# Performance work log

Measured on AMD Instinct MI355X. Metric: run time of the kernel, lower is better.

## Reference

```python
import jax, jax.numpy as jnp
from jax import lax
import numpy as np

B, T, A = 128, 2048, 3
H = 100  # LSTM units
F = 64   # conv filters


def setup_inputs() -> dict:
    key = jax.random.key(0)
    ks = jax.random.split(key, 8)
    s = lambda k, shape, scale: (jax.random.normal(k, shape, dtype=jnp.float32) * scale)
    return {
        "state_input": s(ks[0], (B, T, 1), 1.0),
        "conv_w": s(ks[1], (2, 1, F), 0.5),
        "conv_b": jnp.zeros((F,), jnp.float32),
        "lstm1_w": s(ks[2], (F, 4 * H), 0.08),
        "lstm1_u": s(ks[3], (H, 4 * H), 0.08),
        "lstm1_b": jnp.zeros((4 * H,), jnp.float32),
        "lstm2_w": s(ks[4], (H, 4 * H), 0.08),
        "lstm2_u": s(ks[5], (H, 4 * H), 0.08),
        "lstm2_b": jnp.zeros((4 * H,), jnp.float32),
        "dense_w": s(ks[6], (H, A), 0.1),
        "dense_b": jnp.zeros((A,), jnp.float32),
    }


def _lstm_relu(x, W, U, b, return_sequences):
    # Keras LSTM with activation='relu', recurrent_activation='sigmoid'.
    # Gate order: i, f, g(candidate), o. h = o * relu(c).
    Bz = x.shape[0]
    xz = jnp.einsum("btf,fg->btg", x, W) + b  # precompute input projections [B,T,4H]
    h0 = jnp.zeros((Bz, U.shape[0]), x.dtype)
    c0 = jnp.zeros_like(h0)

    def step(carry, xz_t):
        h, c = carry
        z = xz_t + h @ U
        i, f, g, o = jnp.split(z, 4, axis=-1)
        i = jax.nn.sigmoid(i)
        f = jax.nn.sigmoid(f)
        g = jax.nn.relu(g)
        o = jax.nn.sigmoid(o)
        c = f * c + i * g
        h = o * jax.nn.relu(c)
        return (h, c), (h if return_sequences else 0.0)

    (h_last, _), hs = lax.scan(step, (h0, c0), jnp.swapaxes(xz, 0, 1))
    if return_sequences:
        return jnp.swapaxes(hs, 0, 1)  # [B,T,H]
    return h_last


def reference(state_input, conv_w, conv_b, lstm1_w, lstm1_u, lstm1_b,
              lstm2_w, lstm2_u, lstm2_b, dense_w, dense_b):
    # Conv1D(filters=64, kernel_size=2, padding='valid', relu): [B,T,1]->[B,T-1,64]
    x = lax.conv_general_dilated(
        state_input, conv_w, window_strides=(1,), padding="VALID",
        dimension_numbers=("NWC", "WIO", "NWC"))
    x = jax.nn.relu(x + conv_b)
    # MaxPool1D(pool_size=1) is the identity.
    x = _lstm_relu(x, lstm1_w, lstm1_u, lstm1_b, return_sequences=True)
    # Dropout at inference is identity.
    x = _lstm_relu(x, lstm2_w, lstm2_u, lstm2_b, return_sequences=False)  # [B,H]
    logits = x @ dense_w + dense_b
    return jax.nn.softmax(logits, axis=-1)
```

## Files before the change

### kernel.cpp

```cpp
#include <hip/hip_runtime.h>
#include <math.h>


typedef _Float16 h2 __attribute__((ext_vector_type(2)));

#define TT 2048
#define TP 2047
#define HH 100
#define G4 400
#define FF 64
#define NB 128

#define K1 192
#define QC 112
#define NPH2 (400 * 96)
#define NCH2 (400 * 112)
#define CHK 64
#define NCHUNK 32
#define RINGC 4
#define CHUNK_DW (CHK * 50)

#define WS_FLAGS (NPH2 + NCH2)
#define WS_RING  (WS_FLAGS + 256)

#define L24(X) X(0) X(1) X(2) X(3) X(4) X(5) X(6) X(7) X(8) X(9) \
 X(10) X(11) X(12) X(13) X(14) X(15) X(16) X(17) X(18) X(19) \
 X(20) X(21) X(22) X(23)
#define L28(X) L24(X) X(24) X(25) X(26) X(27)

#define FD(w, x, acc) acc = __builtin_amdgcn_fdot2(w, x, acc, false)
#define B2(f) __builtin_bit_cast(h2, f)

#define DW4(i) h2 wa##i, wb##i, wc##i, wd##i;
#define LPK(i) { const float4 v = gptr[i]; \
  wa##i = B2(v.x); wb##i = B2(v.y); wc##i = B2(v.z); wd##i = B2(v.w); }

#define DOTP(r, i0, i1, i2, i3) { const float4 v = vb[r]; \
  const h2 x0 = B2(v.x), x1 = B2(v.y), x2 = B2(v.z), x3 = B2(v.w); \
  FD(wa##i0, x0, zA0); FD(wb##i0, x0, zB0); FD(wc##i0, x0, zC0); FD(wd##i0, x0, zD0); \
  FD(wa##i1, x1, zA1); FD(wb##i1, x1, zB1); FD(wc##i1, x1, zC1); FD(wd##i1, x1, zD1); \
  FD(wa##i2, x2, zA0); FD(wb##i2, x2, zB0); FD(wc##i2, x2, zC0); FD(wd##i2, x2, zD0); \
  FD(wa##i3, x3, zA1); FD(wb##i3, x3, zB1); FD(wc##i3, x3, zC1); FD(wd##i3, x3, zD1); }

static __device__ __forceinline__ float qsum4(float z) {
    int p1 = __builtin_amdgcn_update_dpp(0, __builtin_bit_cast(int, z),
                                         0xB1, 0xF, 0xF, true);
    float s1 = z + __builtin_bit_cast(float, p1);
    int p2 = __builtin_amdgcn_update_dpp(0, __builtin_bit_cast(int, s1),
                                         0x4E, 0xF, 0xF, true);
    return s1 + __builtin_bit_cast(float, p2);
}
static __device__ __forceinline__ float sig(float z) {
    return 1.0f / (1.0f + __expf(-z));
}

static __device__ __forceinline__ _Float16 pwv(const float* __restrict__ W,
                                               const float* __restrict__ U,
                                               int c, int k) {
    float v = (k < FF) ? W[k * G4 + c] : (k < FF + HH ? U[(k - FF) * G4 + c] : 0.0f);
    return (_Float16)v;
}
static __device__ __forceinline__ _Float16 cwv2(const float* __restrict__ W,
                                                const float* __restrict__ U,
                                                int c, int k) {
    if (k < 112) return (k < HH) ? (_Float16)W[k * G4 + c] : (_Float16)0.0f;
    const int kk = k - 112;
    return (kk < HH) ? (_Float16)U[kk * G4 + c] : (_Float16)0.0f;
}

__global__ void prep_weights(const float* __restrict__ w1, const float* __restrict__ u1,
                             const float* __restrict__ w2, const float* __restrict__ u2,
                             h2* __restrict__ ws)
{
    const int idx = blockIdx.x * 256 + threadIdx.x;
    if (idx >= NPH2 + NCH2) return;
    _Float16 lo, hi;
    if (idx < NPH2) {
        const int rt = idx / 96, r = idx % 96;
        const int q = r >> 2, g = r & 3;
        const int p = rt >> 2, sq = rt & 3;
        const int c = g * HH + p;
        const int k = sq * 48 + 2 * q;
        lo = pwv(w1, u1, c, k); hi = pwv(w1, u1, c, k + 1);
    } else {
        const int j = idx - NPH2;
        const int rt = j / 112, r = j % 112;
        const int i = r >> 2, g = r & 3;
        const int p = rt >> 2, sq = rt & 3;
        const int c = g * HH + p;
        const int k = 56 * sq + 2 * i;
        lo = cwv2(w2, u2, c, k); hi = cwv2(w2, u2, c, k + 1);
    }
    ws[idx] = h2{lo, hi};
}

__global__ __launch_bounds__(512, 2)
void fused_lstm_kernel(const float* __restrict__ s,
                       const float* __restrict__ conv_w,
                       const float* __restrict__ conv_b,
                       const float* __restrict__ b1,
                       const float* __restrict__ b2,
                       const float* __restrict__ dw, const float* __restrict__ db,
                       h2* __restrict__ wpk,
                       float* __restrict__ out)
{
    const int tid  = threadIdx.x;
    const int bb   = blockIdx.x;
    const int b    = bb & (NB - 1);
    const bool prod = bb < NB;

    int* pflag = (int*)(wpk + WS_FLAGS) + b;
    int* aflag = (int*)(wpk + WS_FLAGS) + 128 + b;
    unsigned* ring = (unsigned*)(wpk + WS_RING) + (size_t)b * (RINGC * CHUNK_DW);

    __shared__ float s_buf[TT];
    __shared__ __align__(16) _Float16 X1[2 * K1];
    __shared__ __align__(16) _Float16 CB[CHK * QC];
    __shared__ __align__(16) _Float16 HR[2 * QC];

    if (prod) {
        for (int i = tid; i < TT; i += 512) s_buf[i] = s[(size_t)b * TT + i];
        if (tid < 2 * K1) X1[tid] = (_Float16)0.0f;
    } else {
        if (tid < CHK * 6) {
            const int row = tid / 6, ii = 50 + tid % 6;
            ((unsigned*)CB)[row * 56 + ii] = 0u;
        }
        if (tid < QC) ((unsigned*)HR)[tid] = 0u;
    }
    __syncthreads();

    if (prod) {
        if (tid < 448) {
            const int rt = tid;
            const int active = rt < 400;
            const int lrt = active ? rt : 0;
            const int p = lrt >> 2, sq = lrt & 3;
            const int cA = p, cBi = HH + p, cC = 2 * HH + p, cD = 3 * HH + p;
            const int kb = sq * 48;

            const float4* gptr = (const float4*)(wpk + (size_t)lrt * 96);
            L24(DW4)
            L24(LPK)
            const float bA = b1[cA], bB = b1[cBi], bC = b1[cC], bD = b1[cD];
            __syncthreads();

            float c = 0.0f;
            for (int t = 0; t < TP; ++t) {
                if ((t & 63) == 0) {
                    const int k = t >> 6;
                    if (tid == 0 && k >= RINGC) {
                        int g = 0;
                        while (__hip_atomic_load(aflag, __ATOMIC_ACQUIRE,
                                                 __HIP_MEMORY_SCOPE_AGENT) < k - (RINGC - 1)
                               && g < 50000000) { ++g; __builtin_amdgcn_s_sleep(8); }
                    }
                    __syncthreads();
                }
                if (active) {
                    _Float16* cur = X1 + (t & 1) * K1;
                    _Float16* nx1 = X1 + ((t & 1) ^ 1) * K1;
                    float zA0 = 0.f, zA1 = 0.f, zB0 = 0.f, zB1 = 0.f;
                    float zC0 = 0.f, zC1 = 0.f, zD0 = 0.f, zD1 = 0.f;
                    const float4* vb = (const float4*)(cur + kb);
                    DOTP(0, 0, 1, 2, 3)     DOTP(1, 4, 5, 6, 7)
                    DOTP(2, 8, 9, 10, 11)   DOTP(3, 12, 13, 14, 15)
                    DOTP(4, 16, 17, 18, 19) DOTP(5, 20, 21, 22, 23)
                    const float zi = qsum4(zA0 + zA1) + bA;
                    const float zf = qsum4(zB0 + zB1) + bB;
                    const float zg = qsum4(zC0 + zC1) + bC;
                    const float zo = qsum4(zD0 + zD1) + bD;
                    c = fmaf(sig(zf), c, sig(zi) * fmaxf(zg, 0.f));
                    const float h = sig(zo) * fmaxf(c, 0.f);
                    if (sq == 0) {
                        const _Float16 hq = (_Float16)h;
                        nx1[FF + p] = hq;
                        const unsigned hb = (unsigned)__builtin_bit_cast(unsigned short, hq);
                        const unsigned prt =
                            (unsigned)__builtin_amdgcn_ds_swizzle((int)hb, 0x101F) & 0xFFFFu;
                        if (!(p & 1)) {
                            const unsigned dwv = hb | (prt << 16);
                            __hip_atomic_store(ring + ((t >> 6) & 3) * CHUNK_DW
                                                    + (t & 63) * 50 + (p >> 1),
                                               dwv, __ATOMIC_RELAXED,
                                               __HIP_MEMORY_SCOPE_AGENT);
                        }
                    }
                    if (((t & 63) == 63) || (t == TP - 1))
                        asm volatile("s_waitcnt vmcnt(0)" ::: "memory");
                }
                __syncthreads();
                if (tid == 0 && (((t & 63) == 63) || (t == TP - 1)))
                    __hip_atomic_fetch_add(pflag, 1, __ATOMIC_RELEASE,
                                           __HIP_MEMORY_SCOPE_AGENT);
            }
        } else {
            const int f = tid - 448;
            const float cv0 = conv_w[f], cv1 = conv_w[FF + f], cb0 = conv_b[f];
            X1[f] = (_Float16)fmaxf(fmaf(s_buf[0], cv0, fmaf(s_buf[1], cv1, cb0)), 0.f);
            __syncthreads();
            for (int t = 0; t < TP; ++t) {
                if ((t & 63) == 0) __syncthreads();
                if (t + 1 < TP) {
                    _Float16* nx1 = X1 + ((t & 1) ^ 1) * K1;
                    nx1[f] = (_Float16)fmaxf(
                        fmaf(s_buf[t + 1], cv0, fmaf(s_buf[t + 2], cv1, cb0)), 0.f);
                }
                __syncthreads();
            }
        }
    } else {
        if (tid < 448) {
            const int rt = tid;
            const int active = rt < 400;
            const int lrt = active ? rt : 0;
            const int p = lrt >> 2, sq = lrt & 3;
            const int cA = p, cBi = HH + p, cC = 2 * HH + p, cD = 3 * HH + p;

            const float4* gptr = (const float4*)(wpk + NPH2 + (size_t)lrt * 112);
            L28(DW4)
            L28(LPK)
            const float bA = b2[cA], bB = b2[cBi], bC = b2[cC], bD = b2[cD];
            __syncthreads();

            float c = 0.0f;
            for (int k = 0; k < NCHUNK; ++k) {
                if (tid == 0) {
                    int g = 0;
                    while (__hip_atomic_load(pflag, __ATOMIC_ACQUIRE,
                                             __HIP_MEMORY_SCOPE_AGENT) < k + 1
                           && g < 50000000) { ++g; __builtin_amdgcn_s_sleep(8); }
                }
                __syncthreads();
                const int csz = (TP - (k << 6) < CHK) ? (TP - (k << 6)) : CHK;
                unsigned* gsrc = ring + (k & 3) * CHUNK_DW;
                for (int d = tid; d < csz * 50; d += 448)
                    ((unsigned*)CB)[(d / 50) * 56 + (d % 50)] =
                        __hip_atomic_load(gsrc + d, __ATOMIC_RELAXED,
                                          __HIP_MEMORY_SCOPE_AGENT);
                __syncthreads();
                if (tid == 0)
                    __hip_atomic_fetch_add(aflag, 1, __ATOMIC_RELAXED,
                                           __HIP_MEMORY_SCOPE_AGENT);
                for (int lt = 0; lt < csz; ++lt) {
                    const int t = (k << 6) + lt;
                    if (active) {
                        const _Float16* ob = (sq < 2)
                            ? (CB + lt * QC + sq * 56)
                            : (HR + (t & 1) * QC + (sq - 2) * 56);
                        float zA0 = 0.f, zA1 = 0.f, zB0 = 0.f, zB1 = 0.f;
                        float zC0 = 0.f, zC1 = 0.f, zD0 = 0.f, zD1 = 0.f;
                        const float4* vb = (const float4*)ob;
                        DOTP(0, 0, 1, 2, 3)     DOTP(1, 4, 5, 6, 7)
                        DOTP(2, 8, 9, 10, 11)   DOTP(3, 12, 13, 14, 15)
                        DOTP(4, 16, 17, 18, 19) DOTP(5, 20, 21, 22, 23)
                        DOTP(6, 24, 25, 26, 27)
                        const float zi = qsum4(zA0 + zA1) + bA;
                        const float zf = qsum4(zB0 + zB1) + bB;
                        const float zg = qsum4(zC0 + zC1) + bC;
                        const float zo = qsum4(zD0 + zD1) + bD;
                        c = fmaf(sig(zf), c, sig(zi) * fmaxf(zg, 0.f));
                        const float h = sig(zo) * fmaxf(c, 0.f);
                        if (sq == 0)
                            HR[((t & 1) ^ 1) * QC + p] = (_Float16)h;
                    }
                    __syncthreads();
                }
            }

            if (rt == 0) {
                float l[3];
#pragma unroll
                for (int a = 0; a < 3; ++a) {
                    float acc = db[a];
                    for (int j = 0; j < HH; ++j)
                        acc = fmaf((float)HR[QC + j], dw[j * 3 + a], acc);
                    l[a] = acc;
                }
                const float m = fmaxf(l[0], fmaxf(l[1], l[2]));
                const float e0 = __expf(l[0] - m), e1 = __expf(l[1] - m), e2 = __expf(l[2] - m);
                const float inv = 1.0f / (e0 + e1 + e2);
                out[b * 3 + 0] = e0 * inv;
                out[b * 3 + 1] = e1 * inv;
                out[b * 3 + 2] = e2 * inv;
            }
        } else {
            __syncthreads();
            for (int k = 0; k < NCHUNK; ++k) {
                __syncthreads();
                const int csz = (TP - (k << 6) < CHK) ? (TP - (k << 6)) : CHK;
                __syncthreads();
                for (int lt = 0; lt < csz; ++lt)
                    __syncthreads();
            }
        }
    }
}

extern "C" void kernel_launch(void* const* d_in, const int* in_sizes, int n_in,
                              void* d_out, int out_size, void* d_ws, size_t ws_size,
                              hipStream_t stream) {
    const float* s      = (const float*)d_in[0];
    const float* conv_w = (const float*)d_in[1];
    const float* conv_b = (const float*)d_in[2];
    const float* w1     = (const float*)d_in[3];
    const float* u1     = (const float*)d_in[4];
    const float* b1     = (const float*)d_in[5];
    const float* w2     = (const float*)d_in[6];
    const float* u2     = (const float*)d_in[7];
    const float* b2     = (const float*)d_in[8];
    const float* dw     = (const float*)d_in[9];
    const float* db     = (const float*)d_in[10];

    h2* ws = (h2*)d_ws;
    hipMemsetAsync((void*)((int*)(ws + WS_FLAGS)), 0, 256 * sizeof(int), stream);
    const int nh2 = NPH2 + NCH2;
    prep_weights<<<(nh2 + 255) / 256, 256, 0, stream>>>(w1, u1, w2, u2, ws);
    fused_lstm_kernel<<<256, 512, 0, stream>>>(
        s, conv_w, conv_b, b1, b2, dw, db, ws, (float*)d_out);
}
```

Baseline: 1.879 ms.

## Precompute per-chunk input projections and give each thread one full gate row

Both LSTM layers now compute the input projection for a whole 32-step chunk in parallel into shared memory, leaving only the recurrent h@U dot in the serial loop. Each thread now owns one full gate column instead of a quarter of the K range for four gates, and DPP lane swaps gather the four gate values instead of reducing partial sums. The conv is computed per chunk rather than streamed by a dedicated warp group. In exchange, each thread holds 104 packed weight registers, shared memory grows to about 57 KB, and the chunk size halves, doubling producer/consumer flag handshakes.

Result: slower. 2.371 ms (+26.2%).

```diff
diff --git a/kernel.cpp b/kernel.cpp
--- a/kernel.cpp
+++ b/kernel.cpp
@@ -11,61 +11,31 @@
 #define FF 64
 #define NB 128
 
-#define K1 192
-#define QC 112
-#define NPH2 (400 * 96)
-#define NCH2 (400 * 112)
-#define CHK 64
-#define NCHUNK 32
+#define CHK 32
+#define NCHUNK 64
 #define RINGC 4
 #define CHUNK_DW (CHK * 50)
 
-#define WS_FLAGS (NPH2 + NCH2)
+#define NPW (400 * 84)
+#define NCW (400 * 104)
+#define WS_FLAGS (NPW + NCW)
 #define WS_RING  (WS_FLAGS + 256)
 
-#define L24(X) X(0) X(1) X(2) X(3) X(4) X(5) X(6) X(7) X(8) X(9) \
- X(10) X(11) X(12) X(13) X(14) X(15) X(16) X(17) X(18) X(19) \
- X(20) X(21) X(22) X(23)
-#define L28(X) L24(X) X(24) X(25) X(26) X(27)
-
-#define FD(w, x, acc) acc = __builtin_amdgcn_fdot2(w, x, acc, false)
+#define FD2(w, xs, acc) acc = __builtin_amdgcn_fdot2(w, xs, acc, false)
 #define B2(f) __builtin_bit_cast(h2, f)
 
-#define DW4(i) h2 wa##i, wb##i, wc##i, wd##i;
-#define LPK(i) { const float4 v = gptr[i]; \
-  wa##i = B2(v.x); wb##i = B2(v.y); wc##i = B2(v.z); wd##i = B2(v.w); }
-
-#define DOTP(r, i0, i1, i2, i3) { const float4 v = vb[r]; \
-  const h2 x0 = B2(v.x), x1 = B2(v.y), x2 = B2(v.z), x3 = B2(v.w); \
-  FD(wa##i0, x0, zA0); FD(wb##i0, x0, zB0); FD(wc##i0, x0, zC0); FD(wd##i0, x0, zD0); \
-  FD(wa##i1, x1, zA1); FD(wb##i1, x1, zB1); FD(wc##i1, x1, zC1); FD(wd##i1, x1, zD1); \
-  FD(wa##i2, x2, zA0); FD(wb##i2, x2, zB0); FD(wc##i2, x2, zC0); FD(wd##i2, x2, zD0); \
-  FD(wa##i3, x3, zA1); FD(wb##i3, x3, zB1); FD(wc##i3, x3, zC1); FD(wd##i3, x3, zD1); }
-
-static __device__ __forceinline__ float qsum4(float z) {
-    int p1 = __builtin_amdgcn_update_dpp(0, __builtin_bit_cast(int, z),
-                                         0xB1, 0xF, 0xF, true);
-    float s1 = z + __builtin_bit_cast(float, p1);
-    int p2 = __builtin_amdgcn_update_dpp(0, __builtin_bit_cast(int, s1),
-                                         0x4E, 0xF, 0xF, true);
-    return s1 + __builtin_bit_cast(float, p2);
+static __device__ __forceinline__ float xswap1(float z) {
+    int p = __builtin_amdgcn_update_dpp(0, __builtin_bit_cast(int, z),
+                                        0xB1, 0xF, 0xF, true);
+    return __builtin_bit_cast(float, p);
+}
+static __device__ __forceinline__ float xswap2(float z) {
+    int p = __builtin_amdgcn_update_dpp(0, __builtin_bit_cast(int, z),
+                                        0x4E, 0xF, 0xF, true);
+    return __builtin_bit_cast(float, p);
 }
 static __device__ __forceinline__ float sig(float z) {
     return 1.0f / (1.0f + __expf(-z));
-}
-
-static __device__ __forceinline__ _Float16 pwv(const float* __restrict__ W,
-                                               const float* __restrict__ U,
-                                               int c, int k) {
-    float v = (k < FF) ? W[k * G4 + c] : (k < FF + HH ? U[(k - FF) * G4 + c] : 0.0f);
-    return (_Float16)v;
-}
-static __device__ __forceinline__ _Float16 cwv2(const float* __restrict__ W,
-                                                const float* __restrict__ U,
-                                                int c, int k) {
-    if (k < 112) return (k < HH) ? (_Float16)W[k * G4 + c] : (_Float16)0.0f;
-    const int kk = k - 112;
-    return (kk < HH) ? (_Float16)U[kk * G4 + c] : (_Float16)0.0f;
 }
 
 __global__ void prep_weights(const float* __restrict__ w1, const float* __restrict__ u1,
@@ -73,25 +43,34 @@
                              h2* __restrict__ ws)
 {
     const int idx = blockIdx.x * 256 + threadIdx.x;
-    if (idx >= NPH2 + NCH2) return;
-    _Float16 lo, hi;
-    if (idx < NPH2) {
-        const int rt = idx / 96, r = idx % 96;
-        const int q = r >> 2, g = r & 3;
-        const int p = rt >> 2, sq = rt & 3;
-        const int c = g * HH + p;
-        const int k = sq * 48 + 2 * q;
-        lo = pwv(w1, u1, c, k); hi = pwv(w1, u1, c, k + 1);
+    if (idx >= NPW + NCW) return;
+    float lo = 0.f, hi = 0.f;
+    if (idx < NPW) {
+        const int rt = idx / 84, j = idx % 84;
+        const int c = (rt & 3) * HH + (rt >> 2);
+        if (j < 32) {
+            const int k = 2 * j;
+            lo = w1[k * G4 + c]; hi = w1[(k + 1) * G4 + c];
+        } else {
+            const int kk = 2 * (j - 32);
+            lo = (kk < HH) ? u1[kk * G4 + c] : 0.f;
+            hi = (kk + 1 < HH) ? u1[(kk + 1) * G4 + c] : 0.f;
+        }
     } else {
-        const int j = idx - NPH2;
-        const int rt = j / 112, r = j % 112;
-        const int i = r >> 2, g = r & 3;
-        const int p = rt >> 2, sq = rt & 3;
-        const int c = g * HH + p;
-        const int k = 56 * sq + 2 * i;
-        lo = cwv2(w2, u2, c, k); hi = cwv2(w2, u2, c, k + 1);
-    }
-    ws[idx] = h2{lo, hi};
+        const int i2 = idx - NPW;
+        const int rt = i2 / 104, j = i2 % 104;
+        const int c = (rt & 3) * HH + (rt >> 2);
+        if (j < 52) {
+            const int k = 2 * j;
+            lo = (k < HH) ? w2[k * G4 + c] : 0.f;
+            hi = (k + 1 < HH) ? w2[(k + 1) * G4 + c] : 0.f;
+        } else {
+            const int kk = 2 * (j - 52);
+            lo = (kk < HH) ? u2[kk * G4 + c] : 0.f;
+            hi = (kk + 1 < HH) ? u2[(kk + 1) * G4 + c] : 0.f;
+        }
+    }
+    ws[idx] = h2{(_Float16)lo, (_Float16)hi};
 }
 
 __global__ __launch_bounds__(512, 2)
@@ -113,186 +92,223 @@
     int* aflag = (int*)(wpk + WS_FLAGS) + 128 + b;
     unsigned* ring = (unsigned*)(wpk + WS_RING) + (size_t)b * (RINGC * CHUNK_DW);
 
-    __shared__ float s_buf[TT];
-    __shared__ __align__(16) _Float16 X1[2 * K1];
-    __shared__ __align__(16) _Float16 CB[CHK * QC];
-    __shared__ __align__(16) _Float16 HR[2 * QC];
+    __shared__ __align__(16) unsigned char smem[58368];
+    float*     zs  = (float*)smem;
+    _Float16*  xch = (_Float16*)(smem + 51200);
+    _Float16*  HRp = (_Float16*)(smem + 55296);
+    _Float16*  h1c = (_Float16*)(smem + 51200);
+    _Float16*  HRc = (_Float16*)(smem + 57856);
+
+    const int active = tid < 400;
+    const int lrt = active ? tid : 0;
+    const int gg = tid & 3;
+    const int pp = tid >> 2;
 
     if (prod) {
-        for (int i = tid; i < TT; i += 512) s_buf[i] = s[(size_t)b * TT + i];
-        if (tid < 2 * K1) X1[tid] = (_Float16)0.0f;
+        if (tid < 104) ((unsigned*)HRp)[tid] = 0u;
     } else {
-        if (tid < CHK * 6) {
-            const int row = tid / 6, ii = 50 + tid % 6;
-            ((unsigned*)CB)[row * 56 + ii] = 0u;
-        }
-        if (tid < QC) ((unsigned*)HR)[tid] = 0u;
+        if (tid < 104) ((unsigned*)HRc)[tid] = 0u;
+        if (tid < CHK * 2) {
+            ((unsigned*)h1c)[(tid >> 1) * 52 + 50 + (tid & 1)] = 0u;
+        }
+    }
+
+    h2 gw[52]; h2 uw[52];
+    float bias = 0.f;
+    {
+        const int cidx = (lrt & 3) * HH + (lrt >> 2);
+        if (prod) {
+            const float4* w4 = (const float4*)(wpk + (size_t)lrt * 84);
+#pragma unroll
+            for (int r = 0; r < 8; ++r) {
+                const float4 v = w4[r];
+                gw[4*r+0]=B2(v.x); gw[4*r+1]=B2(v.y); gw[4*r+2]=B2(v.z); gw[4*r+3]=B2(v.w);
+            }
+#pragma unroll
+            for (int r = 0; r < 13; ++r) {
+                const float4 v = w4[8 + r];
+                uw[4*r+0]=B2(v.x); uw[4*r+1]=B2(v.y); uw[4*r+2]=B2(v.z); uw[4*r+3]=B2(v.w);
+            }
+            bias = b1[cidx];
+        } else {
+            const float4* w4 = (const float4*)(wpk + NPW + (size_t)lrt * 104);
+#pragma unroll
+            for (int r = 0; r < 13; ++r) {
+                const float4 v = w4[r];
+                gw[4*r+0]=B2(v.x); gw[4*r+1]=B2(v.y); gw[4*r+2]=B2(v.z); gw[4*r+3]=B2(v.w);
+            }
+#pragma unroll
+            for (int r = 0; r < 13; ++r) {
+                const float4 v = w4[13 + r];
+                uw[4*r+0]=B2(v.x); uw[4*r+1]=B2(v.y); uw[4*r+2]=B2(v.z); uw[4*r+3]=B2(v.w);
+            }
+            bias = b2[cidx];
+        }
+    }
+    float cv0 = 0.f, cv1 = 0.f, cb0 = 0.f;
+    if (prod) {
+        const int f = tid & 63;
+        cv0 = conv_w[f]; cv1 = conv_w[FF + f]; cb0 = conv_b[f];
     }
     __syncthreads();
 
+    float c = 0.0f;
+
     if (prod) {
-        if (tid < 448) {
-            const int rt = tid;
-            const int active = rt < 400;
-            const int lrt = active ? rt : 0;
-            const int p = lrt >> 2, sq = lrt & 3;
-            const int cA = p, cBi = HH + p, cC = 2 * HH + p, cD = 3 * HH + p;
-            const int kb = sq * 48;
-
-            const float4* gptr = (const float4*)(wpk + (size_t)lrt * 96);
-            L24(DW4)
-            L24(LPK)
-            const float bA = b1[cA], bB = b1[cBi], bC = b1[cC], bD = b1[cD];
-            __syncthreads();
-
-            float c = 0.0f;
-            for (int t = 0; t < TP; ++t) {
-                if ((t & 63) == 0) {
-                    const int k = t >> 6;
-                    if (tid == 0 && k >= RINGC) {
-                        int g = 0;
-                        while (__hip_atomic_load(aflag, __ATOMIC_ACQUIRE,
-                                                 __HIP_MEMORY_SCOPE_AGENT) < k - (RINGC - 1)
-                               && g < 50000000) { ++g; __builtin_amdgcn_s_sleep(8); }
-                    }
-                    __syncthreads();
-                }
+        const float* sb = s + (size_t)b * TT;
+        for (int k = 0; k < NCHUNK; ++k) {
+            const int t0  = k * CHK;
+            const int csz = (TP - t0 < CHK) ? (TP - t0) : CHK;
+            if (tid == 0 && k >= RINGC) {
+                int g = 0;
+                while (__hip_atomic_load(aflag, __ATOMIC_ACQUIRE,
+                                         __HIP_MEMORY_SCOPE_AGENT) < k - (RINGC - 1)
+                       && g < 50000000) { ++g; __builtin_amdgcn_s_sleep(8); }
+            }
+#pragma unroll
+            for (int j = 0; j < 4; ++j) {
+                const int e = j * 512 + tid;
+                const int lt = e >> 6, f = e & 63;
+                if (lt < csz) {
+                    const float sv0 = sb[t0 + lt], sv1 = sb[t0 + lt + 1];
+                    xch[lt * 64 + f] =
+                        (_Float16)fmaxf(fmaf(sv0, cv0, fmaf(sv1, cv1, cb0)), 0.f);
+                }
+            }
+            __syncthreads();
+            if (active) {
+                for (int lt = 0; lt < csz; ++lt) {
+                    const float4* xr = (const float4*)(xch + lt * 64);
+                    float za = 0.f, zb = 0.f;
+#pragma unroll
+                    for (int r = 0; r < 8; ++r) {
+                        const float4 v = xr[r];
+                        FD2(gw[4*r+0], B2(v.x), za); FD2(gw[4*r+1], B2(v.y), zb);
+                        FD2(gw[4*r+2], B2(v.z), za); FD2(gw[4*r+3], B2(v.w), zb);
+                    }
+                    zs[lt * 400 + tid] = za + zb;
+                }
+            }
+            __syncthreads();
+            for (int lt = 0; lt < csz; ++lt) {
+                const int t = t0 + lt;
                 if (active) {
-                    _Float16* cur = X1 + (t & 1) * K1;
-                    _Float16* nx1 = X1 + ((t & 1) ^ 1) * K1;
-                    float zA0 = 0.f, zA1 = 0.f, zB0 = 0.f, zB1 = 0.f;
-                    float zC0 = 0.f, zC1 = 0.f, zD0 = 0.f, zD1 = 0.f;
-                    const float4* vb = (const float4*)(cur + kb);
-                    DOTP(0, 0, 1, 2, 3)     DOTP(1, 4, 5, 6, 7)
-                    DOTP(2, 8, 9, 10, 11)   DOTP(3, 12, 13, 14, 15)
-                    DOTP(4, 16, 17, 18, 19) DOTP(5, 20, 21, 22, 23)
-                    const float zi = qsum4(zA0 + zA1) + bA;
-                    const float zf = qsum4(zB0 + zB1) + bB;
-                    const float zg = qsum4(zC0 + zC1) + bC;
-                    const float zo = qsum4(zD0 + zD1) + bD;
+                    const float4* hr4 = (const float4*)(HRp + (t & 1) * 104);
+                    float za = 0.f, zb = 0.f;
+#pragma unroll
+                    for (int r = 0; r < 13; ++r) {
+                        const float4 v = hr4[r];
+                        FD2(uw[4*r+0], B2(v.x), za); FD2(uw[4*r+1], B2(v.y), zb);
+                        FD2(uw[4*r+2], B2(v.z), za); FD2(uw[4*r+3], B2(v.w), zb);
+                    }
+                    const float zown = za + zb + zs[lt * 400 + tid] + bias;
+                    const float v1 = xswap1(zown);
+                    const float v2 = xswap2(zown);
+                    const float v3 = xswap2(v1);
+                    const float zi = gg==0 ? zown : gg==1 ? v1 : gg==2 ? v2 : v3;
+                    const float zf = gg==1 ? zown : gg==0 ? v1 : gg==3 ? v2 : v3;
+                    const float zg = gg==2 ? zown : gg==3 ? v1 : gg==0 ? v2 : v3;
+                    const float zo = gg==3 ? zown : gg==2 ? v1 : gg==1 ? v2 : v3;
                     c = fmaf(sig(zf), c, sig(zi) * fmaxf(zg, 0.f));
                     const float h = sig(zo) * fmaxf(c, 0.f);
-                    if (sq == 0) {
+                    if (gg == 0) {
                         const _Float16 hq = (_Float16)h;
-                        nx1[FF + p] = hq;
+                        HRp[((t & 1) ^ 1) * 104 + pp] = hq;
                         const unsigned hb = (unsigned)__builtin_bit_cast(unsigned short, hq);
                         const unsigned prt =
                             (unsigned)__builtin_amdgcn_ds_swizzle((int)hb, 0x101F) & 0xFFFFu;
-                        if (!(p & 1)) {
-                            const unsigned dwv = hb | (prt << 16);
-                            __hip_atomic_store(ring + ((t >> 6) & 3) * CHUNK_DW
-                                                    + (t & 63) * 50 + (p >> 1),
-                                               dwv, __ATOMIC_RELAXED,
+                        if (!(pp & 1))
+                            __hip_atomic_store(ring + ((t >> 5) & 3) * CHUNK_DW
+                                                    + (t & 31) * 50 + (pp >> 1),
+                                               hb | (prt << 16), __ATOMIC_RELAXED,
                                                __HIP_MEMORY_SCOPE_AGENT);
-                        }
-                    }
-                    if (((t & 63) == 63) || (t == TP - 1))
-                        asm volatile("s_waitcnt vmcnt(0)" ::: "memory");
+                    }
                 }
                 __syncthreads();
-                if (tid == 0 && (((t & 63) == 63) || (t == TP - 1)))
-                    __hip_atomic_fetch_add(pflag, 1, __ATOMIC_RELEASE,
-                                           __HIP_MEMORY_SCOPE_AGENT);
-            }
-        } else {
-            const int f = tid - 448;
-            const float cv0 = conv_w[f], cv1 = conv_w[FF + f], cb0 = conv_b[f];
-            X1[f] = (_Float16)fmaxf(fmaf(s_buf[0], cv0, fmaf(s_buf[1], cv1, cb0)), 0.f);
-            __syncthreads();
-            for (int t = 0; t < TP; ++t) {
-                if ((t & 63) == 0) __syncthreads();
-                if (t + 1 < TP) {
-                    _Float16* nx1 = X1 + ((t & 1) ^ 1) * K1;
-                    nx1[f] = (_Float16)fmaxf(
-                        fmaf(s_buf[t + 1], cv0, fmaf(s_buf[t + 2], cv1, cb0)), 0.f);
+            }
+            asm volatile("s_waitcnt vmcnt(0)" ::: "memory");
+            __syncthreads();
+            if (tid == 0)
+                __hip_atomic_fetch_add(pflag, 1, __ATOMIC_RELEASE,
+                                       __HIP_MEMORY_SCOPE_AGENT);
+        }
+    } else {
+        for (int k = 0; k < NCHUNK; ++k) {
+            const int t0  = k * CHK;
+            const int csz = (TP - t0 < CHK) ? (TP - t0) : CHK;
+            if (tid == 0) {
+                int g = 0;
+                while (__hip_atomic_load(pflag, __ATOMIC_ACQUIRE,
+                                         __HIP_MEMORY_SCOPE_AGENT) < k + 1
+                       && g < 50000000) { ++g; __builtin_amdgcn_s_sleep(8); }
+            }
+            __syncthreads();
+            unsigned* gsrc = ring + (k & 3) * CHUNK_DW;
+            for (int d = tid; d < csz * 50; d += 512)
+                ((unsigned*)h1c)[(d / 50) * 52 + (d % 50)] =
+                    __hip_atomic_load(gsrc + d, __ATOMIC_RELAXED,
+                                      __HIP_MEMORY_SCOPE_AGENT);
+            __syncthreads();
+            if (tid == 0)
+                __hip_atomic_fetch_add(aflag, 1, __ATOMIC_RELAXED,
+                                       __HIP_MEMORY_SCOPE_AGENT);
+            if (active) {
+                for (int lt = 0; lt < csz; ++lt) {
+                    const float4* xr = (const float4*)(h1c + lt * 104);
+                    float za = 0.f, zb = 0.f;
+#pragma unroll
+                    for (int r = 0; r < 13; ++r) {
+                        const float4 v = xr[r];
+                        FD2(gw[4*r+0], B2(v.x), za); FD2(gw[4*r+1], B2(v.y), zb);
+                        FD2(gw[4*r+2], B2(v.z), za); FD2(gw[4*r+3], B2(v.w), zb);
+                    }
+                    zs[lt * 400 + tid] = za + zb;
+                }
+            }
+            __syncthreads();
+            for (int lt = 0; lt < csz; ++lt) {
+                const int t = t0 + lt;
+                if (active) {
+                    const float4* hr4 = (const float4*)(HRc + (t & 1) * 104);
+                    float za = 0.f, zb = 0.f;
+#pragma unroll
+                    for (int r = 0; r < 13; ++r) {
+                        const float4 v = hr4[r];
+                        FD2(uw[4*r+0], B2(v.x), za); FD2(uw[4*r+1], B2(v.y), zb);
+                        FD2(uw[4*r+2], B2(v.z), za); FD2(uw[4*r+3], B2(v.w), zb);
+                    }
+                    const float zown = za + zb + zs[lt * 400 + tid] + bias;
+                    const float v1 = xswap1(zown);
+                    const float v2 = xswap2(zown);
+                    const float v3 = xswap2(v1);
+                    const float zi = gg==0 ? zown : gg==1 ? v1 : gg==2 ? v2 : v3;
+                    const float zf = gg==1 ? zown : gg==0 ? v1 : gg==3 ? v2 : v3;
+                    const float zg = gg==2 ? zown : gg==3 ? v1 : gg==0 ? v2 : v3;
+                    const float zo = gg==3 ? zown : gg==2 ? v1 : gg==1 ? v2 : v3;
+                    c = fmaf(sig(zf), c, sig(zi) * fmaxf(zg, 0.f));
+                    const float h = sig(zo) * fmaxf(c, 0.f);
+                    if (gg == 0)
+                        HRc[((t & 1) ^ 1) * 104 + pp] = (_Float16)h;
                 }
                 __syncthreads();
             }
         }
-    } else {
-        if (tid < 448) {
-            const int rt = tid;
-            const int active = rt < 400;
-            const int lrt = active ? rt : 0;
-            const int p = lrt >> 2, sq = lrt & 3;
-            const int cA = p, cBi = HH + p, cC = 2 * HH + p, cD = 3 * HH + p;
-
-            const float4* gptr = (const float4*)(wpk + NPH2 + (size_t)lrt * 112);
-            L28(DW4)
-            L28(LPK)
-            const float bA = b2[cA], bB = b2[cBi], bC = b2[cC], bD = b2[cD];
-            __syncthreads();
-
-            float c = 0.0f;
-            for (int k = 0; k < NCHUNK; ++k) {
-                if (tid == 0) {
-                    int g = 0;
-                    while (__hip_atomic_load(pflag, __ATOMIC_ACQUIRE,
-                                             __HIP_MEMORY_SCOPE_AGENT) < k + 1
-                           && g < 50000000) { ++g; __builtin_amdgcn_s_sleep(8); }
-                }
-                __syncthreads();
-                const int csz = (TP - (k << 6) < CHK) ? (TP - (k << 6)) : CHK;
-                unsigned* gsrc = ring + (k & 3) * CHUNK_DW;
-                for (int d = tid; d < csz * 50; d += 448)
-                    ((unsigned*)CB)[(d / 50) * 56 + (d % 50)] =
-                        __hip_atomic_load(gsrc + d, __ATOMIC_RELAXED,
-                                          __HIP_MEMORY_SCOPE_AGENT);
-                __syncthreads();
-                if (tid == 0)
-                    __hip_atomic_fetch_add(aflag, 1, __ATOMIC_RELAXED,
-                                           __HIP_MEMORY_SCOPE_AGENT);
-                for (int lt = 0; lt < csz; ++lt) {
-                    const int t = (k << 6) + lt;
-                    if (active) {
-                        const _Float16* ob = (sq < 2)
-                            ? (CB + lt * QC + sq * 56)
-                            : (HR + (t & 1) * QC + (sq - 2) * 56);
-                        float zA0 = 0.f, zA1 = 0.f, zB0 = 0.f, zB1 = 0.f;
-                        float zC0 = 0.f, zC1 = 0.f, zD0 = 0.f, zD1 = 0.f;
-                        const float4* vb = (const float4*)ob;
-                        DOTP(0, 0, 1, 2, 3)     DOTP(1, 4, 5, 6, 7)
-                        DOTP(2, 8, 9, 10, 11)   DOTP(3, 12, 13, 14, 15)
-                        DOTP(4, 16, 17, 18, 19) DOTP(5, 20, 21, 22, 23)
-                        DOTP(6, 24, 25, 26, 27)
-                        const float zi = qsum4(zA0 + zA1) + bA;
-                        const float zf = qsum4(zB0 + zB1) + bB;
-                        const float zg = qsum4(zC0 + zC1) + bC;
-                        const float zo = qsum4(zD0 + zD1) + bD;
-                        c = fmaf(sig(zf), c, sig(zi) * fmaxf(zg, 0.f));
-                        const float h = sig(zo) * fmaxf(c, 0.f);
-                        if (sq == 0)
-                            HR[((t & 1) ^ 1) * QC + p] = (_Float16)h;
-                    }
-                    __syncthreads();
-                }
-            }
-
-            if (rt == 0) {
-                float l[3];
-#pragma unroll
-                for (int a = 0; a < 3; ++a) {
-                    float acc = db[a];
-                    for (int j = 0; j < HH; ++j)
-                        acc = fmaf((float)HR[QC + j], dw[j * 3 + a], acc);
-                    l[a] = acc;
-                }
-                const float m = fmaxf(l[0], fmaxf(l[1], l[2]));
-                const float e0 = __expf(l[0] - m), e1 = __expf(l[1] - m), e2 = __expf(l[2] - m);
-                const float inv = 1.0f / (e0 + e1 + e2);
-                out[b * 3 + 0] = e0 * inv;
-                out[b * 3 + 1] = e1 * inv;
-                out[b * 3 + 2] = e2 * inv;
-            }
-        } else {
-            __syncthreads();
-            for (int k = 0; k < NCHUNK; ++k) {
-                __syncthreads();
-                const int csz = (TP - (k << 6) < CHK) ? (TP - (k << 6)) : CHK;
-                __syncthreads();
-                for (int lt = 0; lt < csz; ++lt)
-                    __syncthreads();
-            }
+
+        if (tid == 0) {
+            float l[3];
+#pragma unroll
+            for (int a = 0; a < 3; ++a) {
+                float acc = db[a];
+                for (int j = 0; j < HH; ++j)
+                    acc = fmaf((float)HRc[104 + j], dw[j * 3 + a], acc);
+                l[a] = acc;
+            }
+            const float m = fmaxf(l[0], fmaxf(l[1], l[2]));
+            const float e0 = __expf(l[0] - m), e1 = __expf(l[1] - m), e2 = __expf(l[2] - m);
+            const float inv = 1.0f / (e0 + e1 + e2);
+            out[b * 3 + 0] = e0 * inv;
+            out[b * 3 + 1] = e1 * inv;
+            out[b * 3 + 2] = e2 * inv;
         }
     }
 }
@@ -314,7 +330,7 @@
 
     h2* ws = (h2*)d_ws;
     hipMemsetAsync((void*)((int*)(ws + WS_FLAGS)), 0, 256 * sizeof(int), stream);
-    const int nh2 = NPH2 + NCH2;
+    const int nh2 = NPW + NCW;
     prep_weights<<<(nh2 + 255) / 256, 256, 0, stream>>>(w1, u1, w2, u2, ws);
     fused_lstm_kernel<<<256, 512, 0, stream>>>(
         s, conv_w, conv_b, b1, b2, dw, db, ws, (float*)d_out);
```

## Repartition LSTM gate work into two gates by two K-halves per lane quad

Applied to the files above, without the earlier changes.

Each group of four lanes now splits the work as two gate pairs times two halves of the reduction dimension, where before each lane took one K-quarter of all four gates. This cuts padding in the packed weights (88 and 100 h2 per lane instead of 96 and 112) and replaces the 4-way DPP reduction with a 2-way sum plus a cross-swap to gather all gates. The h layout in X1 is interleaved to match the new split, and the CB and HR row strides shrink accordingly. The cost is extra select logic and a more intricate index mapping, which is easy to get wrong.

Result: no change. 1.857 ms (-1.2%).

```diff
diff --git a/kernel.cpp b/kernel.cpp
--- a/kernel.cpp
+++ b/kernel.cpp
@@ -11,61 +11,33 @@
 #define FF 64
 #define NB 128
 
-#define K1 192
-#define QC 112
-#define NPH2 (400 * 96)
-#define NCH2 (400 * 112)
+#define X1R 176
+#define CBQ 104
+#define NPW (400 * 88)
+#define NCW (400 * 100)
 #define CHK 64
 #define NCHUNK 32
 #define RINGC 4
 #define CHUNK_DW (CHK * 50)
 
-#define WS_FLAGS (NPH2 + NCH2)
+#define WS_FLAGS (NPW + NCW)
 #define WS_RING  (WS_FLAGS + 256)
 
-#define L24(X) X(0) X(1) X(2) X(3) X(4) X(5) X(6) X(7) X(8) X(9) \
- X(10) X(11) X(12) X(13) X(14) X(15) X(16) X(17) X(18) X(19) \
- X(20) X(21) X(22) X(23)
-#define L28(X) L24(X) X(24) X(25) X(26) X(27)
-
-#define FD(w, x, acc) acc = __builtin_amdgcn_fdot2(w, x, acc, false)
+#define FD2(w, xs, acc) acc = __builtin_amdgcn_fdot2(w, xs, acc, false)
 #define B2(f) __builtin_bit_cast(h2, f)
 
-#define DW4(i) h2 wa##i, wb##i, wc##i, wd##i;
-#define LPK(i) { const float4 v = gptr[i]; \
-  wa##i = B2(v.x); wb##i = B2(v.y); wc##i = B2(v.z); wd##i = B2(v.w); }
-
-#define DOTP(r, i0, i1, i2, i3) { const float4 v = vb[r]; \
-  const h2 x0 = B2(v.x), x1 = B2(v.y), x2 = B2(v.z), x3 = B2(v.w); \
-  FD(wa##i0, x0, zA0); FD(wb##i0, x0, zB0); FD(wc##i0, x0, zC0); FD(wd##i0, x0, zD0); \
-  FD(wa##i1, x1, zA1); FD(wb##i1, x1, zB1); FD(wc##i1, x1, zC1); FD(wd##i1, x1, zD1); \
-  FD(wa##i2, x2, zA0); FD(wb##i2, x2, zB0); FD(wc##i2, x2, zC0); FD(wd##i2, x2, zD0); \
-  FD(wa##i3, x3, zA1); FD(wb##i3, x3, zB1); FD(wc##i3, x3, zC1); FD(wd##i3, x3, zD1); }
-
-static __device__ __forceinline__ float qsum4(float z) {
-    int p1 = __builtin_amdgcn_update_dpp(0, __builtin_bit_cast(int, z),
-                                         0xB1, 0xF, 0xF, true);
-    float s1 = z + __builtin_bit_cast(float, p1);
-    int p2 = __builtin_amdgcn_update_dpp(0, __builtin_bit_cast(int, s1),
-                                         0x4E, 0xF, 0xF, true);
-    return s1 + __builtin_bit_cast(float, p2);
+static __device__ __forceinline__ float psum2(float z) {
+    int p = __builtin_amdgcn_update_dpp(0, __builtin_bit_cast(int, z),
+                                        0xB1, 0xF, 0xF, true);
+    return z + __builtin_bit_cast(float, p);
+}
+static __device__ __forceinline__ float xswap2(float z) {
+    int p = __builtin_amdgcn_update_dpp(0, __builtin_bit_cast(int, z),
+                                        0x4E, 0xF, 0xF, true);
+    return __builtin_bit_cast(float, p);
 }
 static __device__ __forceinline__ float sig(float z) {
     return 1.0f / (1.0f + __expf(-z));
-}
-
-static __device__ __forceinline__ _Float16 pwv(const float* __restrict__ W,
-                                               const float* __restrict__ U,
-                                               int c, int k) {
-    float v = (k < FF) ? W[k * G4 + c] : (k < FF + HH ? U[(k - FF) * G4 + c] : 0.0f);
-    return (_Float16)v;
-}
-static __device__ __forceinline__ _Float16 cwv2(const float* __restrict__ W,
-                                                const float* __restrict__ U,
-                                                int c, int k) {
-    if (k < 112) return (k < HH) ? (_Float16)W[k * G4 + c] : (_Float16)0.0f;
-    const int kk = k - 112;
-    return (kk < HH) ? (_Float16)U[kk * G4 + c] : (_Float16)0.0f;
 }
 
 __global__ void prep_weights(const float* __restrict__ w1, const float* __restrict__ u1,
@@ -73,25 +45,38 @@
                              h2* __restrict__ ws)
 {
     const int idx = blockIdx.x * 256 + threadIdx.x;
-    if (idx >= NPH2 + NCH2) return;
-    _Float16 lo, hi;
-    if (idx < NPH2) {
-        const int rt = idx / 96, r = idx % 96;
-        const int q = r >> 2, g = r & 3;
-        const int p = rt >> 2, sq = rt & 3;
-        const int c = g * HH + p;
-        const int k = sq * 48 + 2 * q;
-        lo = pwv(w1, u1, c, k); hi = pwv(w1, u1, c, k + 1);
+    if (idx >= NPW + NCW) return;
+    float lo = 0.f, hi = 0.f;
+    if (idx < NPW) {
+        const int rt = idx / 88, r = idx % 88;
+        const int qq = (r >> 2) * 2 + ((r & 3) >> 1);
+        const int gs = r & 1;
+        const int p = rt >> 2, g2 = (rt >> 1) & 1, kh = rt & 1;
+        const int col = (2 * g2 + gs) * HH + p;
+        const int E0 = 2 * qq;
+#pragma unroll
+        for (int e = 0; e < 2; ++e) {
+            const int E = E0 + e;
+            float v = 0.f;
+            if (E < 82) {
+                const int k = kh * 82 + E;
+                v = (k < FF) ? w1[k * G4 + col] : u1[(k - FF) * G4 + col];
+            }
+            if (e == 0) lo = v; else hi = v;
+        }
     } else {
-        const int j = idx - NPH2;
-        const int rt = j / 112, r = j % 112;
-        const int i = r >> 2, g = r & 3;
-        const int p = rt >> 2, sq = rt & 3;
-        const int c = g * HH + p;
-        const int k = 56 * sq + 2 * i;
-        lo = cwv2(w2, u2, c, k); hi = cwv2(w2, u2, c, k + 1);
+        const int i2 = idx - NPW;
+        const int rt = i2 / 100, r = i2 % 100;
+        const int qq = (r >> 2) * 2 + ((r & 3) >> 1);
+        const int gs = r & 1;
+        const int p = rt >> 2, g2 = (rt >> 1) & 1, kh = rt & 1;
+        const int col = (2 * g2 + gs) * HH + p;
+        const int k0 = 2 * qq;
+        const float* M = kh ? u2 : w2;
+        lo = M[k0 * G4 + col];
+        hi = M[(k0 + 1) * G4 + col];
     }
-    ws[idx] = h2{lo, hi};
+    ws[idx] = h2{(_Float16)lo, (_Float16)hi};
 }
 
 __global__ __launch_bounds__(512, 2)
@@ -114,19 +99,17 @@
     unsigned* ring = (unsigned*)(wpk + WS_RING) + (size_t)b * (RINGC * CHUNK_DW);
 
     __shared__ float s_buf[TT];
-    __shared__ __align__(16) _Float16 X1[2 * K1];
-    __shared__ __align__(16) _Float16 CB[CHK * QC];
-    __shared__ __align__(16) _Float16 HR[2 * QC];
+    __shared__ __align__(16) _Float16 X1[2 * X1R];
+    __shared__ __align__(16) _Float16 CB[CHK * CBQ];
+    __shared__ __align__(16) _Float16 HR[2 * CBQ];
 
     if (prod) {
         for (int i = tid; i < TT; i += 512) s_buf[i] = s[(size_t)b * TT + i];
-        if (tid < 2 * K1) X1[tid] = (_Float16)0.0f;
+        if (tid < X1R) ((unsigned*)X1)[tid] = 0u;
     } else {
-        if (tid < CHK * 6) {
-            const int row = tid / 6, ii = 50 + tid % 6;
-            ((unsigned*)CB)[row * 56 + ii] = 0u;
-        }
-        if (tid < QC) ((unsigned*)HR)[tid] = 0u;
+        if (tid < CBQ) ((unsigned*)HR)[tid] = 0u;
+        if (tid < CHK * 2)
+            ((unsigned*)CB)[(tid >> 1) * 52 + 50 + (tid & 1)] = 0u;
     }
     __syncthreads();
 
@@ -135,14 +118,23 @@
             const int rt = tid;
             const int active = rt < 400;
             const int lrt = active ? rt : 0;
-            const int p = lrt >> 2, sq = lrt & 3;
-            const int cA = p, cBi = HH + p, cC = 2 * HH + p, cD = 3 * HH + p;
-            const int kb = sq * 48;
-
-            const float4* gptr = (const float4*)(wpk + (size_t)lrt * 96);
-            L24(DW4)
-            L24(LPK)
-            const float bA = b1[cA], bB = b1[cBi], bC = b1[cC], bD = b1[cD];
+            const int p  = lrt >> 2;
+            const int g2 = (lrt >> 1) & 1;
+            const int kh = lrt & 1;
+            const int cL = (2 * g2) * HH + p;
+
+            h2 wa[44], wb[44];
+            {
+                const float4* w4 = (const float4*)(wpk + (size_t)lrt * 88);
+#pragma unroll
+                for (int j = 0; j < 22; ++j) {
+                    const float4 v = w4[j];
+                    wa[2*j]   = B2(v.x); wb[2*j]   = B2(v.y);
+                    wa[2*j+1] = B2(v.z); wb[2*j+1] = B2(v.w);
+                }
+            }
+            const float bL = b1[cL], bH = b1[cL + HH];
+            const int hoff = (p < 18) ? (64 + p) : (p + 70);
             __syncthreads();
 
             float c = 0.0f;
@@ -158,33 +150,38 @@
                     __syncthreads();
                 }
                 if (active) {
-                    _Float16* cur = X1 + (t & 1) * K1;
-                    _Float16* nx1 = X1 + ((t & 1) ^ 1) * K1;
-                    float zA0 = 0.f, zA1 = 0.f, zB0 = 0.f, zB1 = 0.f;
-                    float zC0 = 0.f, zC1 = 0.f, zD0 = 0.f, zD1 = 0.f;
-                    const float4* vb = (const float4*)(cur + kb);
-                    DOTP(0, 0, 1, 2, 3)     DOTP(1, 4, 5, 6, 7)
-                    DOTP(2, 8, 9, 10, 11)   DOTP(3, 12, 13, 14, 15)
-                    DOTP(4, 16, 17, 18, 19) DOTP(5, 20, 21, 22, 23)
-                    const float zi = qsum4(zA0 + zA1) + bA;
-                    const float zf = qsum4(zB0 + zB1) + bB;
-                    const float zg = qsum4(zC0 + zC1) + bC;
-                    const float zo = qsum4(zD0 + zD1) + bD;
+                    _Float16* cur = X1 + (t & 1) * X1R;
+                    _Float16* nx1 = X1 + ((t & 1) ^ 1) * X1R;
+                    float za0 = 0.f, za1 = 0.f, zb0 = 0.f, zb1 = 0.f;
+                    const float4* vb = (const float4*)(cur + kh * 88);
+#pragma unroll
+                    for (int r2 = 0; r2 < 11; ++r2) {
+                        const float4 v = vb[r2];
+                        FD2(wa[4*r2+0], B2(v.x), za0); FD2(wb[4*r2+0], B2(v.x), zb0);
+                        FD2(wa[4*r2+1], B2(v.y), za1); FD2(wb[4*r2+1], B2(v.y), zb1);
+                        FD2(wa[4*r2+2], B2(v.z), za0); FD2(wb[4*r2+2], B2(v.z), zb0);
+                        FD2(wa[4*r2+3], B2(v.w), za1); FD2(wb[4*r2+3], B2(v.w), zb1);
+                    }
+                    const float zaS = psum2(za0 + za1) + bL;
+                    const float zbS = psum2(zb0 + zb1) + bH;
+                    const float oa = xswap2(zaS), ob = xswap2(zbS);
+                    const float zi = g2 ? oa  : zaS;
+                    const float zf = g2 ? ob  : zbS;
+                    const float zg = g2 ? zaS : oa;
+                    const float zo = g2 ? zbS : ob;
                     c = fmaf(sig(zf), c, sig(zi) * fmaxf(zg, 0.f));
                     const float h = sig(zo) * fmaxf(c, 0.f);
-                    if (sq == 0) {
+                    if ((rt & 3) == 0) {
                         const _Float16 hq = (_Float16)h;
-                        nx1[FF + p] = hq;
+                        nx1[hoff] = hq;
                         const unsigned hb = (unsigned)__builtin_bit_cast(unsigned short, hq);
                         const unsigned prt =
                             (unsigned)__builtin_amdgcn_ds_swizzle((int)hb, 0x101F) & 0xFFFFu;
-                        if (!(p & 1)) {
-                            const unsigned dwv = hb | (prt << 16);
+                        if (!(p & 1))
                             __hip_atomic_store(ring + ((t >> 6) & 3) * CHUNK_DW
                                                     + (t & 63) * 50 + (p >> 1),
-                                               dwv, __ATOMIC_RELAXED,
+                                               hb | (prt << 16), __ATOMIC_RELAXED,
                                                __HIP_MEMORY_SCOPE_AGENT);
-                        }
                     }
                     if (((t & 63) == 63) || (t == TP - 1))
                         asm volatile("s_waitcnt vmcnt(0)" ::: "memory");
@@ -202,7 +199,7 @@
             for (int t = 0; t < TP; ++t) {
                 if ((t & 63) == 0) __syncthreads();
                 if (t + 1 < TP) {
-                    _Float16* nx1 = X1 + ((t & 1) ^ 1) * K1;
+                    _Float16* nx1 = X1 + ((t & 1) ^ 1) * X1R;
                     nx1[f] = (_Float16)fmaxf(
                         fmaf(s_buf[t + 1], cv0, fmaf(s_buf[t + 2], cv1, cb0)), 0.f);
                 }
@@ -214,13 +211,22 @@
             const int rt = tid;
             const int active = rt < 400;
             const int lrt = active ? rt : 0;
-            const int p = lrt >> 2, sq = lrt & 3;
-            const int cA = p, cBi = HH + p, cC = 2 * HH + p, cD = 3 * HH + p;
-
-            const float4* gptr = (const float4*)(wpk + NPH2 + (size_t)lrt * 112);
-            L28(DW4)
-            L28(LPK)
-            const float bA = b2[cA], bB = b2[cBi], bC = b2[cC], bD = b2[cD];
+            const int p  = lrt >> 2;
+            const int g2 = (lrt >> 1) & 1;
+            const int kh = lrt & 1;
+            const int cL = (2 * g2) * HH + p;
+
+            h2 wa[50], wb[50];
+            {
+                const float4* w4 = (const float4*)(wpk + NPW + (size_t)lrt * 100);
+#pragma unroll
+                for (int j = 0; j < 25; ++j) {
+                    const float4 v = w4[j];
+                    wa[2*j]   = B2(v.x); wb[2*j]   = B2(v.y);
+                    wa[2*j+1] = B2(v.z); wb[2*j+1] = B2(v.w);
+                }
+            }
+            const float bL = b2[cL], bH = b2[cL + HH];
             __syncthreads();
 
             float c = 0.0f;
@@ -235,7 +241,7 @@
                 const int csz = (TP - (k << 6) < CHK) ? (TP - (k << 6)) : CHK;
                 unsigned* gsrc = ring + (k & 3) * CHUNK_DW;
                 for (int d = tid; d < csz * 50; d += 448)
-                    ((unsigned*)CB)[(d / 50) * 56 + (d % 50)] =
+                    ((unsigned*)CB)[(d / 50) * 52 + (d % 50)] =
                         __hip_atomic_load(gsrc + d, __ATOMIC_RELAXED,
                                           __HIP_MEMORY_SCOPE_AGENT);
                 __syncthreads();
@@ -245,24 +251,34 @@
                 for (int lt = 0; lt < csz; ++lt) {
                     const int t = (k << 6) + lt;
                     if (active) {
-                        const _Float16* ob = (sq < 2)
-                            ? (CB + lt * QC + sq * 56)
-                            : (HR + (t & 1) * QC + (sq - 2) * 56);
-                        float zA0 = 0.f, zA1 = 0.f, zB0 = 0.f, zB1 = 0.f;
-                        float zC0 = 0.f, zC1 = 0.f, zD0 = 0.f, zD1 = 0.f;
-                        const float4* vb = (const float4*)ob;
-                        DOTP(0, 0, 1, 2, 3)     DOTP(1, 4, 5, 6, 7)
-                        DOTP(2, 8, 9, 10, 11)   DOTP(3, 12, 13, 14, 15)
-                        DOTP(4, 16, 17, 18, 19) DOTP(5, 20, 21, 22, 23)
-                        DOTP(6, 24, 25, 26, 27)
-                        const float zi = qsum4(zA0 + zA1) + bA;
-                        const float zf = qsum4(zB0 + zB1) + bB;
-                        const float zg = qsum4(zC0 + zC1) + bC;
-                        const float zo = qsum4(zD0 + zD1) + bD;
+                        const _Float16* base = kh ? (HR + (t & 1) * CBQ)
+                                                  : (CB + lt * CBQ);
+                        float za0 = 0.f, za1 = 0.f, zb0 = 0.f, zb1 = 0.f;
+                        const float4* vb = (const float4*)base;
+#pragma unroll
+                        for (int r2 = 0; r2 < 12; ++r2) {
+                            const float4 v = vb[r2];
+                            FD2(wa[4*r2+0], B2(v.x), za0); FD2(wb[4*r2+0], B2(v.x), zb0);
+                            FD2(wa[4*r2+1], B2(v.y), za1); FD2(wb[4*r2+1], B2(v.y), zb1);
+                            FD2(wa[4*r2+2], B2(v.z), za0); FD2(wb[4*r2+2], B2(v.z), zb0);
+                            FD2(wa[4*r2+3], B2(v.w), za1); FD2(wb[4*r2+3], B2(v.w), zb1);
+                        }
+                        {
+                            const float2 tv = *(const float2*)(base + 96);
+                            FD2(wa[48], B2(tv.x), za0); FD2(wb[48], B2(tv.x), zb0);
+                            FD2(wa[49], B2(tv.y), za1); FD2(wb[49], B2(tv.y), zb1);
+                        }
+                        const float zaS = psum2(za0 + za1) + bL;
+                        const float zbS = psum2(zb0 + zb1) + bH;
+                        const float oa = xswap2(zaS), ob = xswap2(zbS);
+                        const float zi = g2 ? oa  : zaS;
+                        const float zf = g2 ? ob  : zbS;
+                        const float zg = g2 ? zaS : oa;
+                        const float zo = g2 ? zbS : ob;
                         c = fmaf(sig(zf), c, sig(zi) * fmaxf(zg, 0.f));
                         const float h = sig(zo) * fmaxf(c, 0.f);
-                        if (sq == 0)
-                            HR[((t & 1) ^ 1) * QC + p] = (_Float16)h;
+                        if ((rt & 3) == 0)
+                            HR[((t & 1) ^ 1) * CBQ + p] = (_Float16)h;
                     }
                     __syncthreads();
                 }
@@ -274,7 +290,7 @@
                 for (int a = 0; a < 3; ++a) {
                     float acc = db[a];
                     for (int j = 0; j < HH; ++j)
-                        acc = fmaf((float)HR[QC + j], dw[j * 3 + a], acc);
+                        acc = fmaf((float)HR[CBQ + j], dw[j * 3 + a], acc);
                     l[a] = acc;
                 }
                 const float m = fmaxf(l[0], fmaxf(l[1], l[2]));
@@ -314,7 +330,7 @@
 
     h2* ws = (h2*)d_ws;
     hipMemsetAsync((void*)((int*)(ws + WS_FLAGS)), 0, 256 * sizeof(int), stream);
-    const int nh2 = NPH2 + NCH2;
+    const int nh2 = NPW + NCW;
     prep_weights<<<(nh2 + 255) / 256, 256, 0, stream>>>(w1, u1, w2, u2, ws);
     fused_lstm_kernel<<<256, 512, 0, stream>>>(
         s, conv_w, conv_b, b1, b2, dw, db, ws, (float*)d_out);
```
